# Optimization experiments

Measured on AMD Instinct MI355X. Metric: run time of the kernel, lower is better.

## Reference

```python
import jax, jax.numpy as jnp
import numpy as np

HIDDEN = 2560
NUM_HEADS = 8
NUM_KV_HEADS = 1
HEAD_DIM = 512  # is_full=True -> HEAD_DIM_FULL
MAX_HD = 512
SCALE = 1.0 / float(HEAD_DIM) ** 0.5
SEQ = 32768
SLIDE = 512
CUR_POS = 4000
RING_POS = 100


def setup_inputs() -> dict:
    key = jax.random.key(0)
    ks = jax.random.split(key, 7)
    x = jax.random.normal(ks[0], (1, HIDDEN, 1, 1), jnp.float32)
    kv_full = jax.random.normal(ks[1], (2, NUM_KV_HEADS, SEQ, MAX_HD), jnp.float32) * 0.02
    kv_sliding = jax.random.normal(ks[2], (2, NUM_KV_HEADS, SLIDE, MAX_HD), jnp.float32) * 0.02
    wq = jax.random.normal(ks[3], (NUM_HEADS * HEAD_DIM, HIDDEN), jnp.float32) * 0.02
    wk = jax.random.normal(ks[4], (NUM_KV_HEADS * HEAD_DIM, HIDDEN), jnp.float32) * 0.02
    wv = jax.random.normal(ks[5], (NUM_KV_HEADS * HEAD_DIM, HIDDEN), jnp.float32) * 0.02
    wo = jax.random.normal(ks[6], (HIDDEN, NUM_HEADS * HEAD_DIM), jnp.float32) * 0.02
    return {"x": x, "kv_sliding": kv_sliding, "kv_full": kv_full,
            "wq": wq, "wk": wk, "wv": wv, "wo": wo,
            "current_pos": CUR_POS, "ring_pos": RING_POS}


def reference(x, kv_sliding, kv_full, wq, wk, wv, wo, current_pos, ring_pos):
    # 1x1 convs on a [1,C,1,1] input are plain matvecs
    xv = x.reshape(HIDDEN)
    q = (wq @ xv).reshape(NUM_HEADS, HEAD_DIM)            # [H, D]
    k = (wk @ xv).reshape(NUM_KV_HEADS, HEAD_DIM)         # [1, D]
    v = (wv @ xv).reshape(NUM_KV_HEADS, HEAD_DIM)         # [1, D]
    # is_full=True, slot_idx=0: slice-update write into kv_full at current_pos
    kv_full = jax.lax.dynamic_update_slice(
        kv_full, k[None, :, None, :].astype(kv_full.dtype), (0, 0, current_pos, 0))
    kv_full = jax.lax.dynamic_update_slice(
        kv_full, v[None, :, None, :].astype(kv_full.dtype), (1, 0, current_pos, 0))
    k_cache = kv_full[0, 0, :, :HEAD_DIM]                 # [S, D]
    v_cache = kv_full[1, 0, :, :HEAD_DIM]                 # [S, D]
    # GQA with 1 kv head: repeat == broadcast across the H query heads
    scores = jnp.einsum('hd,sd->hs', q.astype(jnp.float32),
                        k_cache.astype(jnp.float32)) * SCALE   # [H, S]
    probs = jax.nn.softmax(scores, axis=-1)
    attn = jnp.einsum('hs,sd->hd', probs,
                      v_cache.astype(jnp.float32)).astype(x.dtype)  # [H, D]
    out = (wo @ attn.reshape(NUM_HEADS * HEAD_DIM)).reshape(1, HIDDEN, 1, 1)
    return out
```

## Files before the change

kernel.cpp:

```cpp
#include <hip/hip_runtime.h>
#include <stdint.h>

#define HIDDEN 2560
#define NHEADS 8
#define HD 512
#define QDIM (NHEADS * HD)
#define SEQ 32768
#define CHUNK 64
#define NCHUNK (SEQ / CHUNK)
#define PART_ST (8 + NHEADS * HD)
#define SCALE 0.044194173824159216f

#define WS_QKV 0
#define WS_K   4096
#define WS_V   4608
#define WS_ATT 8192
#define WS_PART 16384

__global__ __launch_bounds__(256) void qkv_gemv(
    const float* __restrict__ x,
    const float* __restrict__ wq,
    const float* __restrict__ wk,
    const float* __restrict__ wv,
    float* __restrict__ qkv) {
  const int row = blockIdx.x * 4 + (threadIdx.x >> 6);
  const int lane = threadIdx.x & 63;
  const float* w;
  if (row < QDIM) w = wq + (size_t)row * HIDDEN;
  else if (row < QDIM + HD) w = wk + (size_t)(row - QDIM) * HIDDEN;
  else w = wv + (size_t)(row - QDIM - HD) * HIDDEN;
  float acc = 0.f;
#pragma unroll
  for (int i = 0; i < 5; i++) {
    const int j = i * 512 + lane * 8;
    float4 a0 = *(const float4*)(w + j);
    float4 a1 = *(const float4*)(w + j + 4);
    float4 b0 = *(const float4*)(x + j);
    float4 b1 = *(const float4*)(x + j + 4);
    acc += a0.x * b0.x + a0.y * b0.y + a0.z * b0.z + a0.w * b0.w +
           a1.x * b1.x + a1.y * b1.y + a1.z * b1.z + a1.w * b1.w;
  }
#pragma unroll
  for (int off = 32; off > 0; off >>= 1) acc += __shfl_xor(acc, off);
  if (lane == 0) qkv[row] = acc;
}

__global__ __launch_bounds__(256) void attn_partial(
    const float* __restrict__ kvfull,
    const float* __restrict__ ws,
    const int* __restrict__ cur_pos,
    float* __restrict__ part) {
  __shared__ float accbuf[4][NHEADS * HD];
  __shared__ float denbuf[4][NHEADS];
  const int tid = threadIdx.x;
  const int lane = tid & 63;
  const int wid = tid >> 6;
  const int cur = cur_pos[0];
  const int s0 = blockIdx.x * CHUNK + wid * 16;
  const float* K = kvfull;
  const float* V = kvfull + (size_t)SEQ * HD;

  float qf[NHEADS][8];
#pragma unroll
  for (int h = 0; h < NHEADS; h++) {
    float4 a = *(const float4*)(ws + WS_QKV + h * HD + lane * 8);
    float4 b = *(const float4*)(ws + WS_QKV + h * HD + lane * 8 + 4);
    qf[h][0] = a.x; qf[h][1] = a.y; qf[h][2] = a.z; qf[h][3] = a.w;
    qf[h][4] = b.x; qf[h][5] = b.y; qf[h][6] = b.z; qf[h][7] = b.w;
  }

  float acc[NHEADS][8];
#pragma unroll
  for (int h = 0; h < NHEADS; h++)
#pragma unroll
    for (int e = 0; e < 8; e++) acc[h][e] = 0.f;
  float den[NHEADS];
#pragma unroll
  for (int h = 0; h < NHEADS; h++) den[h] = 0.f;

#pragma unroll 2
  for (int u = 0; u < 16; u++) {
    const int s = s0 + u;
    const float* kr = (s == cur) ? (ws + WS_K) : (K + (size_t)s * HD);
    const float* vr = (s == cur) ? (ws + WS_V) : (V + (size_t)s * HD);
    float4 k0 = *(const float4*)(kr + lane * 8);
    float4 k1 = *(const float4*)(kr + lane * 8 + 4);
    float4 v0 = *(const float4*)(vr + lane * 8);
    float4 v1 = *(const float4*)(vr + lane * 8 + 4);
    const float kb[8] = {k0.x, k0.y, k0.z, k0.w, k1.x, k1.y, k1.z, k1.w};
    float p[NHEADS];
#pragma unroll
    for (int h = 0; h < NHEADS; h++) {
      float t = 0.f;
#pragma unroll
      for (int e = 0; e < 8; e++) t += kb[e] * qf[h][e];
      p[h] = t;
    }
#pragma unroll
    for (int off = 32; off > 0; off >>= 1) {
#pragma unroll
      for (int h = 0; h < NHEADS; h++) p[h] += __shfl_xor(p[h], off);
    }
#pragma unroll
    for (int h = 0; h < NHEADS; h++) {
      const float pe = __expf(p[h] * SCALE);
      den[h] += pe;
      acc[h][0] += pe * v0.x; acc[h][1] += pe * v0.y;
      acc[h][2] += pe * v0.z; acc[h][3] += pe * v0.w;
      acc[h][4] += pe * v1.x; acc[h][5] += pe * v1.y;
      acc[h][6] += pe * v1.z; acc[h][7] += pe * v1.w;
    }
  }

#pragma unroll
  for (int h = 0; h < NHEADS; h++) {
    float4 lo = make_float4(acc[h][0], acc[h][1], acc[h][2], acc[h][3]);
    float4 hi = make_float4(acc[h][4], acc[h][5], acc[h][6], acc[h][7]);
    *(float4*)(&accbuf[wid][h * HD + lane * 8])     = lo;
    *(float4*)(&accbuf[wid][h * HD + lane * 8 + 4]) = hi;
  }
  if (lane == 0) {
#pragma unroll
    for (int h = 0; h < NHEADS; h++) denbuf[wid][h] = den[h];
  }
  __syncthreads();

  float* pb = part + (size_t)blockIdx.x * PART_ST;
  if (tid < NHEADS)
    pb[tid] = denbuf[0][tid] + denbuf[1][tid] + denbuf[2][tid] + denbuf[3][tid];
  for (int i = tid; i < QDIM / 4; i += 256) {
    float4 a = *(float4*)(&accbuf[0][i * 4]);
    float4 b = *(float4*)(&accbuf[1][i * 4]);
    float4 c = *(float4*)(&accbuf[2][i * 4]);
    float4 d = *(float4*)(&accbuf[3][i * 4]);
    a.x += b.x + c.x + d.x; a.y += b.y + c.y + d.y;
    a.z += b.z + c.z + d.z; a.w += b.w + c.w + d.w;
    *(float4*)(pb + 8 + i * 4) = a;
  }
}

__global__ __launch_bounds__(256) void attn_reduce(
    const float* __restrict__ part,
    float* __restrict__ attn) {
  const int h = blockIdx.x >> 4;
  const int dgrp = blockIdx.x & 15;
  const int tid = threadIdx.x;
  __shared__ float red[256];
  __shared__ float pacc[8][32];

  red[tid] = part[(size_t)tid * PART_ST + h] + part[(size_t)(tid + 256) * PART_ST + h];
  __syncthreads();
  for (int off = 128; off > 0; off >>= 1) {
    if (tid < off) red[tid] += red[tid + off];
    __syncthreads();
  }
  const float Linv = 1.f / red[0];

  const int dloc = tid & 31;
  const int bs = tid >> 5;
  const int d = dgrp * 32 + dloc;
  float acc = 0.f;
#pragma unroll 8
  for (int b = bs * (NCHUNK / 8); b < (bs + 1) * (NCHUNK / 8); b++) {
    acc += part[(size_t)b * PART_ST + 8 + h * HD + d];
  }
  pacc[bs][dloc] = acc;
  __syncthreads();
  if (tid < 32) {
    float s = ((pacc[0][tid] + pacc[1][tid]) + (pacc[2][tid] + pacc[3][tid])) +
              ((pacc[4][tid] + pacc[5][tid]) + (pacc[6][tid] + pacc[7][tid]));
    attn[h * HD + dgrp * 32 + tid] = s * Linv;
  }
}

__global__ __launch_bounds__(256) void out_gemv(
    const float* __restrict__ wo,
    const float* __restrict__ attn,
    float* __restrict__ out) {
  const int row = blockIdx.x * 4 + (threadIdx.x >> 6);
  const int lane = threadIdx.x & 63;
  const float* w = wo + (size_t)row * QDIM;
  float acc = 0.f;
#pragma unroll
  for (int i = 0; i < 8; i++) {
    const int j = i * 512 + lane * 8;
    float4 w0 = *(const float4*)(w + j);
    float4 w1 = *(const float4*)(w + j + 4);
    float4 a0 = *(const float4*)(attn + j);
    float4 a1 = *(const float4*)(attn + j + 4);
    acc += w0.x * a0.x + w0.y * a0.y + w0.z * a0.z + w0.w * a0.w +
           w1.x * a1.x + w1.y * a1.y + w1.z * a1.z + w1.w * a1.w;
  }
#pragma unroll
  for (int off = 32; off > 0; off >>= 1) acc += __shfl_xor(acc, off);
  if (lane == 0) out[row] = acc;
}

extern "C" void kernel_launch(void* const* d_in, const int* in_sizes, int n_in,
                              void* d_out, int out_size, void* d_ws, size_t ws_size,
                              hipStream_t stream) {
  (void)in_sizes; (void)n_in; (void)out_size; (void)ws_size;
  const float* x      = (const float*)d_in[0];
  const float* kvfull = (const float*)d_in[2];
  const float* wq     = (const float*)d_in[3];
  const float* wk     = (const float*)d_in[4];
  const float* wv     = (const float*)d_in[5];
  const float* wo     = (const float*)d_in[6];
  const int* cur_pos  = (const int*)d_in[7];
  float* out = (float*)d_out;
  float* ws = (float*)d_ws;

  qkv_gemv<<<(QDIM + 2 * HD) / 4, 256, 0, stream>>>(x, wq, wk, wv, ws + WS_QKV);
  attn_partial<<<NCHUNK, 256, 0, stream>>>(kvfull, ws, cur_pos, ws + WS_PART);
  attn_reduce<<<NHEADS * 16, 256, 0, stream>>>(ws + WS_PART, ws + WS_ATT);
  out_gemv<<<HIDDEN / 4, 256, 0, stream>>>(wo, ws + WS_ATT, out);
}
```

Before: 280.4 us.

## Prefetch next K/V row in registers and shrink LDS reduction buffer

The attention partial kernel now loads the next sequence row's K and V into registers while it computes on the current row, so global-load latency overlaps the dot products and exp work. The per-block cross-wave reduction is also split into four passes of two heads each, which cuts the shared buffer from 64 KB to 16 KB and may let more blocks share a CU. In exchange it adds about 16 live registers and extra __syncthreads barriers in the epilogue, and the higher register pressure could cap occupancy instead.

```diff
diff --git a/kernel.cpp b/kernel.cpp
--- a/kernel.cpp
+++ b/kernel.cpp
@@ -50,7 +50,7 @@
     const float* __restrict__ ws,
     const int* __restrict__ cur_pos,
     float* __restrict__ part) {
-  __shared__ float accbuf[4][NHEADS * HD];
+  __shared__ float accbuf[4][2 * HD];
   __shared__ float denbuf[4][NHEADS];
   const int tid = threadIdx.x;
   const int lane = tid & 63;
@@ -78,15 +78,24 @@
 #pragma unroll
   for (int h = 0; h < NHEADS; h++) den[h] = 0.f;
 
-#pragma unroll 2
+  const float* kr0 = (s0 == cur) ? (ws + WS_K) : (K + (size_t)s0 * HD);
+  const float* vr0 = (s0 == cur) ? (ws + WS_V) : (V + (size_t)s0 * HD);
+  float4 k0 = *(const float4*)(kr0 + lane * 8);
+  float4 k1 = *(const float4*)(kr0 + lane * 8 + 4);
+  float4 v0 = *(const float4*)(vr0 + lane * 8);
+  float4 v1 = *(const float4*)(vr0 + lane * 8 + 4);
+
   for (int u = 0; u < 16; u++) {
-    const int s = s0 + u;
-    const float* kr = (s == cur) ? (ws + WS_K) : (K + (size_t)s * HD);
-    const float* vr = (s == cur) ? (ws + WS_V) : (V + (size_t)s * HD);
-    float4 k0 = *(const float4*)(kr + lane * 8);
-    float4 k1 = *(const float4*)(kr + lane * 8 + 4);
-    float4 v0 = *(const float4*)(vr + lane * 8);
-    float4 v1 = *(const float4*)(vr + lane * 8 + 4);
+    float4 nk0, nk1, nv0, nv1;
+    if (u < 15) {
+      const int sn = s0 + u + 1;
+      const float* krn = (sn == cur) ? (ws + WS_K) : (K + (size_t)sn * HD);
+      const float* vrn = (sn == cur) ? (ws + WS_V) : (V + (size_t)sn * HD);
+      nk0 = *(const float4*)(krn + lane * 8);
+      nk1 = *(const float4*)(krn + lane * 8 + 4);
+      nv0 = *(const float4*)(vrn + lane * 8);
+      nv1 = *(const float4*)(vrn + lane * 8 + 4);
+    }
     const float kb[8] = {k0.x, k0.y, k0.z, k0.w, k1.x, k1.y, k1.z, k1.w};
     float p[NHEADS];
 #pragma unroll
@@ -110,33 +119,42 @@
       acc[h][4] += pe * v1.x; acc[h][5] += pe * v1.y;
       acc[h][6] += pe * v1.z; acc[h][7] += pe * v1.w;
     }
-  }
-
-#pragma unroll
-  for (int h = 0; h < NHEADS; h++) {
-    float4 lo = make_float4(acc[h][0], acc[h][1], acc[h][2], acc[h][3]);
-    float4 hi = make_float4(acc[h][4], acc[h][5], acc[h][6], acc[h][7]);
-    *(float4*)(&accbuf[wid][h * HD + lane * 8])     = lo;
-    *(float4*)(&accbuf[wid][h * HD + lane * 8 + 4]) = hi;
-  }
+    k0 = nk0; k1 = nk1; v0 = nv0; v1 = nv1;
+  }
+
   if (lane == 0) {
 #pragma unroll
     for (int h = 0; h < NHEADS; h++) denbuf[wid][h] = den[h];
   }
-  __syncthreads();
 
   float* pb = part + (size_t)blockIdx.x * PART_ST;
+#pragma unroll
+  for (int r = 0; r < 4; r++) {
+    const int h0 = r * 2;
+#pragma unroll
+    for (int hh = 0; hh < 2; hh++) {
+      float4 lo = make_float4(acc[h0 + hh][0], acc[h0 + hh][1],
+                              acc[h0 + hh][2], acc[h0 + hh][3]);
+      float4 hi = make_float4(acc[h0 + hh][4], acc[h0 + hh][5],
+                              acc[h0 + hh][6], acc[h0 + hh][7]);
+      *(float4*)(&accbuf[wid][hh * HD + lane * 8])     = lo;
+      *(float4*)(&accbuf[wid][hh * HD + lane * 8 + 4]) = hi;
+    }
+    __syncthreads();
+    {
+      const int i = tid * 4;
+      float4 a = *(float4*)(&accbuf[0][i]);
+      float4 b = *(float4*)(&accbuf[1][i]);
+      float4 c = *(float4*)(&accbuf[2][i]);
+      float4 d = *(float4*)(&accbuf[3][i]);
+      a.x += b.x + c.x + d.x; a.y += b.y + c.y + d.y;
+      a.z += b.z + c.z + d.z; a.w += b.w + c.w + d.w;
+      *(float4*)(pb + 8 + h0 * HD + i) = a;
+    }
+    __syncthreads();
+  }
   if (tid < NHEADS)
     pb[tid] = denbuf[0][tid] + denbuf[1][tid] + denbuf[2][tid] + denbuf[3][tid];
-  for (int i = tid; i < QDIM / 4; i += 256) {
-    float4 a = *(float4*)(&accbuf[0][i * 4]);
-    float4 b = *(float4*)(&accbuf[1][i * 4]);
-    float4 c = *(float4*)(&accbuf[2][i * 4]);
-    float4 d = *(float4*)(&accbuf[3][i * 4]);
-    a.x += b.x + c.x + d.x; a.y += b.y + c.y + d.y;
-    a.z += b.z + c.z + d.z; a.w += b.w + c.w + d.w;
-    *(float4*)(pb + 8 + i * 4) = a;
-  }
 }
 
 __global__ __launch_bounds__(256) void attn_reduce(
```

After: 279.6 us. About the same (-0.3%).
